# Kernel tuning notes

Measured on AMD Instinct MI355X. Metric: run time of the kernel, lower is better.

The kernel has to match this reference:

```python
import jax, jax.numpy as jnp
import numpy as np

EPS = 1e-6
NUM_HEADS = 16


def _layernorm(x, g, b):
    m = jnp.mean(x, axis=-1, keepdims=True)
    v = jnp.mean(jnp.square(x - m), axis=-1, keepdims=True)
    return (x - m) / jnp.sqrt(v + EPS) * g + b


def _rotate_half(x):
    x1, x2 = jnp.split(x, 2, axis=-1)
    return jnp.concatenate([-x2, x1], axis=-1)


def setup_inputs() -> dict:
    key = jax.random.key(0)
    B, N, C = 2, 2048, 1024
    H = NUM_HEADS
    D = C // H
    F = int(C * 4.0)
    ks = jax.random.split(key, 12)
    s = 0.02
    pos = jnp.arange(N)[:, None].astype(jnp.float32)
    inv_freq = 1.0 / (10000.0 ** (jnp.arange(0, D, 2, dtype=jnp.float32) / D))
    freqs = pos * inv_freq[None, :]          # [N, D/2]
    emb = jnp.concatenate([freqs, freqs], axis=-1)  # [N, D]
    return {
        "x": jax.random.normal(ks[0], (B, N, C), jnp.float32),
        "rotary_cos": jnp.cos(emb),
        "rotary_sin": jnp.sin(emb),
        "ln1_g": jnp.ones((C,), jnp.float32),
        "ln1_b": jnp.zeros((C,), jnp.float32),
        "Wq": jax.random.normal(ks[1], (C, C), jnp.float32) * s,
        "bq": jnp.zeros((C,), jnp.float32),
        "Wk": jax.random.normal(ks[2], (C, C), jnp.float32) * s,
        "bk": jnp.zeros((C,), jnp.float32),
        "Wv": jax.random.normal(ks[3], (C, C), jnp.float32) * s,
        "bv": jnp.zeros((C,), jnp.float32),
        "Wo": jax.random.normal(ks[4], (C, C), jnp.float32) * s,
        "bo": jnp.zeros((C,), jnp.float32),
        "ln2_g": jnp.ones((C,), jnp.float32),
        "ln2_b": jnp.zeros((C,), jnp.float32),
        "W1": jax.random.normal(ks[5], (F, C), jnp.float32) * s,
        "b1": jnp.zeros((F,), jnp.float32),
        "W2": jax.random.normal(ks[6], (C, F), jnp.float32) * s,
        "b2": jnp.zeros((C,), jnp.float32),
    }


def reference(x, rotary_cos, rotary_sin, ln1_g, ln1_b, Wq, bq, Wk, bk, Wv, bv,
              Wo, bo, ln2_g, ln2_b, W1, b1, W2, b2):
    B, N, C = x.shape
    H = NUM_HEADS
    D = C // H

    # --- attention branch ---
    h = _layernorm(x, ln1_g, ln1_b)
    q = (h @ Wq.T + bq).reshape(B, N, H, D).transpose(0, 2, 1, 3)  # [B,H,N,D]
    k = (h @ Wk.T + bk).reshape(B, N, H, D).transpose(0, 2, 1, 3)
    v = (h @ Wv.T + bv).reshape(B, N, H, D).transpose(0, 2, 1, 3)

    cos = rotary_cos[None, None, :, :]  # [1,1,N,D]
    sin = rotary_sin[None, None, :, :]
    q = q * cos + _rotate_half(q) * sin
    k = k * cos + _rotate_half(k) * sin

    scale = D ** -0.5
    attn = jnp.einsum('bhnd,bhmd->bhnm', q, k) * scale
    attn = jax.nn.softmax(attn, axis=-1)
    out = jnp.einsum('bhnm,bhmd->bhnd', attn, v)
    out = out.transpose(0, 2, 1, 3).reshape(B, N, C)
    out = out @ Wo.T + bo
    x = x + out

    # --- MLP branch ---
    h = _layernorm(x, ln2_g, ln2_b)
    h = jax.nn.gelu(h @ W1.T + b1, approximate=False)  # torch nn.GELU exact
    h = h @ W2.T + b2
    return x + h
```

## Files before the change

kernel.cpp:

```cpp
#include <hip/hip_runtime.h>
#include <hip/hip_bf16.h>

#define B_ 2
#define N_ 2048
#define C_ 1024
#define H_ 16
#define D_ 64
#define F_ 4096
#define M_ 4096

typedef __attribute__((ext_vector_type(8))) short bf16x8;
typedef __attribute__((ext_vector_type(4))) float f32x4;

__device__ inline unsigned short f2bf(float f) {
  unsigned int u = __float_as_uint(f);
  u = (u + 0x7FFFu + ((u >> 16) & 1u)) >> 16;
  return (unsigned short)u;
}
__device__ inline float bf2f(unsigned short u) {
  unsigned int x = ((unsigned int)u) << 16;
  return __uint_as_float(x);
}

__global__ __launch_bounds__(256)
void cvt_all(const float4* __restrict__ s0, const float4* __restrict__ s1,
             const float4* __restrict__ s2, const float4* __restrict__ s3,
             const float4* __restrict__ s4, const float4* __restrict__ s5,
             ushort4* __restrict__ d0, ushort4* __restrict__ d1,
             ushort4* __restrict__ d2, ushort4* __restrict__ d3,
             ushort4* __restrict__ d4, ushort4* __restrict__ d5) {
  int b = blockIdx.x;
  const float4* s; ushort4* d; int i;
  if      (b < 1024) { s = s0; d = d0; i = b * 256 + threadIdx.x; }
  else if (b < 2048) { s = s1; d = d1; i = (b - 1024) * 256 + threadIdx.x; }
  else if (b < 3072) { s = s2; d = d2; i = (b - 2048) * 256 + threadIdx.x; }
  else if (b < 4096) { s = s3; d = d3; i = (b - 3072) * 256 + threadIdx.x; }
  else if (b < 8192) { s = s4; d = d4; i = (b - 4096) * 256 + threadIdx.x; }
  else               { s = s5; d = d5; i = (b - 8192) * 256 + threadIdx.x; }
  float4 f = s[i];
  ushort4 o;
  o.x = f2bf(f.x); o.y = f2bf(f.y); o.z = f2bf(f.z); o.w = f2bf(f.w);
  d[i] = o;
}

__global__ __launch_bounds__(256)
void ln_kernel(const float* __restrict__ x, const float* __restrict__ g,
               const float* __restrict__ b, unsigned short* __restrict__ out) {
  __shared__ float red[8];
  const int row = blockIdx.x;
  const int t = threadIdx.x;
  const float4 xv = *(const float4*)(x + row * 1024 + t * 4);
  float s  = xv.x + xv.y + xv.z + xv.w;
  float sq = xv.x * xv.x + xv.y * xv.y + xv.z * xv.z + xv.w * xv.w;
  #pragma unroll
  for (int off = 32; off >= 1; off >>= 1) {
    s  += __shfl_down(s, off);
    sq += __shfl_down(sq, off);
  }
  const int lane = t & 63, wave = t >> 6;
  if (lane == 0) { red[wave * 2] = s; red[wave * 2 + 1] = sq; }
  __syncthreads();
  float ts = red[0] + red[2] + red[4] + red[6];
  float tq = red[1] + red[3] + red[5] + red[7];
  float mean = ts * (1.0f / 1024.0f);
  float var  = tq * (1.0f / 1024.0f) - mean * mean;
  float rstd = rsqrtf(var + 1e-6f);
  float xs[4] = {xv.x, xv.y, xv.z, xv.w};
  #pragma unroll
  for (int i = 0; i < 4; i++) {
    int c = t * 4 + i;
    float y = (xs[i] - mean) * rstd * g[c] + b[c];
    out[row * 1024 + c] = f2bf(y);
  }
}

__global__ __launch_bounds__(256)
void add_bias(const float* __restrict__ resid, const float* __restrict__ bias,
              float* __restrict__ out) {
  const int i = (blockIdx.x * 256 + threadIdx.x) * 4;
  const int col = i & 1023;
  float4 r = *(const float4*)(resid + i);
  float4 b = *(const float4*)(bias + col);
  float4 o;
  o.x = r.x + b.x; o.y = r.y + b.y; o.z = r.z + b.z; o.w = r.w + b.w;
  *(float4*)(out + i) = o;
}

__global__ __launch_bounds__(512, 1)
void gemm_splitk(const unsigned short* __restrict__ A,
                 const unsigned short* __restrict__ Bw,
                 int Kfull, int ksplit,
                 float* __restrict__ out) {
  __shared__ unsigned short sA[2][256 * 64];
  __shared__ unsigned short sB[2][128 * 64];
  const int t = threadIdx.x;
  const int wave = t >> 6, lane = t & 63;
  const int quad = lane >> 4, l16 = lane & 15;
  const int wm = (wave >> 1) * 64, wn = (wave & 1) * 64;
  const int id = blockIdx.x;
  const int xcd = id & 7, r_ = id >> 3;
  const int m_blk = xcd * 2 + (r_ & 1);
  const int cu = r_ >> 1;
  const int n_blk = cu & 7;
  const int split = cu >> 3;
  const int m0 = m_blk * 256, n0 = n_blk * 128;
  const int k0base = split * ksplit;

  f32x4 acc[4][4];
  #pragma unroll
  for (int i = 0; i < 4; i++)
    #pragma unroll
    for (int j = 0; j < 4; j++) acc[i][j] = (f32x4){0.f, 0.f, 0.f, 0.f};

  const int sc = (((t & 7) ^ ((t >> 3) & 7)) * 8);
  const unsigned short* gA = A  + (long)(m0 + (t >> 3)) * Kfull + k0base + sc;
  const unsigned short* gB = Bw + (long)(n0 + (t >> 3)) * Kfull + k0base + sc;

  auto stage_pair = [&](int k0, int buf, int pr) {
    if (pr < 2) {
      #pragma unroll
      for (int i = pr * 2; i < pr * 2 + 2; i++)
        __builtin_amdgcn_global_load_lds((const unsigned int*)(gA + (long)(64 * i) * Kfull + k0),
                                         (unsigned int*)(&sA[buf][i * 4096 + wave * 8 * 64]), 16, 0, 0);
    } else {
      #pragma unroll
      for (int i = 0; i < 2; i++)
        __builtin_amdgcn_global_load_lds((const unsigned int*)(gB + (long)(64 * i) * Kfull + k0),
                                         (unsigned int*)(&sB[buf][i * 4096 + wave * 8 * 64]), 16, 0, 0);
    }
  };

  stage_pair(0, 0, 0); stage_pair(0, 0, 1); stage_pair(0, 0, 2);
  stage_pair(64, 1, 0);
  asm volatile("s_waitcnt vmcnt(2)" ::: "memory");
  __builtin_amdgcn_s_barrier();

  const int so0 = ((quad ^ (l16 & 7)) * 8);
  const int so1 = (((4 + quad) ^ (l16 & 7)) * 8);

  const int nk = ksplit >> 6;
  for (int t_ = 0; t_ < nk; t_++) {
    const int R = t_ & 1;
    const unsigned short* rA = sA[R];
    const unsigned short* rB = sB[R];
    {
      bf16x8 af[4], bfr[4];
      #pragma unroll
      for (int ii = 0; ii < 4; ii++)
        af[ii] = *(const bf16x8*)(&rA[(wm + ii * 16 + l16) * 64 + so0]);
      #pragma unroll
      for (int j = 0; j < 4; j++)
        bfr[j] = *(const bf16x8*)(&rB[(wn + j * 16 + l16) * 64 + so0]);
      if (t_ + 1 < nk) stage_pair((t_ + 1) * 64, R ^ 1, 1);
      __builtin_amdgcn_s_barrier();
      asm volatile("s_waitcnt lgkmcnt(0)" ::: "memory");
      __builtin_amdgcn_sched_barrier(0);
      __builtin_amdgcn_s_setprio(1);
      #pragma unroll
      for (int ii = 0; ii < 4; ii++)
        #pragma unroll
        for (int j = 0; j < 4; j++)
          acc[ii][j] = __builtin_amdgcn_mfma_f32_16x16x32_bf16(af[ii], bfr[j], acc[ii][j], 0, 0, 0);
      __builtin_amdgcn_s_setprio(0);
      __builtin_amdgcn_s_barrier();
    }
    {
      bf16x8 af[4], bfr[4];
      #pragma unroll
      for (int ii = 0; ii < 4; ii++)
        af[ii] = *(const bf16x8*)(&rA[(wm + ii * 16 + l16) * 64 + so1]);
      #pragma unroll
      for (int j = 0; j < 4; j++)
        bfr[j] = *(const bf16x8*)(&rB[(wn + j * 16 + l16) * 64 + so1]);
      if (t_ + 1 < nk) stage_pair((t_ + 1) * 64, R ^ 1, 2);
      __builtin_amdgcn_s_barrier();
      asm volatile("s_waitcnt lgkmcnt(0)" ::: "memory");
      __builtin_amdgcn_sched_barrier(0);
      __builtin_amdgcn_s_setprio(1);
      #pragma unroll
      for (int ii = 0; ii < 4; ii++)
        #pragma unroll
        for (int j = 0; j < 4; j++)
          acc[ii][j] = __builtin_amdgcn_mfma_f32_16x16x32_bf16(af[ii], bfr[j], acc[ii][j], 0, 0, 0);
      __builtin_amdgcn_s_setprio(0);
    }
    __builtin_amdgcn_s_barrier();
    if (t_ + 2 < nk) {
      stage_pair((t_ + 2) * 64, R, 0);
      asm volatile("s_waitcnt vmcnt(2)" ::: "memory");
      __builtin_amdgcn_s_barrier();
    } else if (t_ + 1 < nk) {
      asm volatile("s_waitcnt vmcnt(0)" ::: "memory");
      __builtin_amdgcn_s_barrier();
    }
  }

  #pragma unroll
  for (int ii = 0; ii < 4; ii++) {
    #pragma unroll
    for (int j = 0; j < 4; j++) {
      int col = n0 + wn + j * 16 + l16;
      #pragma unroll
      for (int r = 0; r < 4; r++) {
        int row = m0 + wm + ii * 16 + quad * 4 + r;
        unsafeAtomicAdd(&out[row * 1024 + col], acc[ii][j][r]);
      }
    }
  }
}

template<int EPI>
__global__ __launch_bounds__(512, 1)
void gemm256(const unsigned short* __restrict__ A,
             const unsigned short* __restrict__ Bw,
             const float* __restrict__ bias,
             const float* __restrict__ bq, const float* __restrict__ bk,
             const float* __restrict__ bv,
             const float* __restrict__ rc, const float* __restrict__ rs,
             unsigned short* __restrict__ o0,
             unsigned short* __restrict__ ko, unsigned short* __restrict__ vt) {
  const int K = 1024;
  __shared__ unsigned short sA[2][256 * 64];
  __shared__ unsigned short sB[2][256 * 64];
  const int t = threadIdx.x;
  const int wave = t >> 6, lane = t & 63;
  const int quad = lane >> 4, l16 = lane & 15;
  const int wm = (wave & 1) * 128, wn = (wave >> 1) * 64;
  const int id = blockIdx.x;
  const int xcd = id & 7, r_ = id >> 3;
  int m_blk, n_blk;
  if (EPI == 0) { n_blk = xcd * 2 + (r_ >> 4); m_blk = r_ & 15; }
  else          { m_blk = xcd * 2 + r_ / 12;   n_blk = r_ % 12; }
  const int m0 = m_blk * 256, n0 = n_blk * 256;

  f32x4 acc[8][4];
  #pragma unroll
  for (int i = 0; i < 8; i++)
    #pragma unroll
    for (int j = 0; j < 4; j++) acc[i][j] = (f32x4){0.f, 0.f, 0.f, 0.f};

  const int sc = (((t & 7) ^ ((t >> 3) & 7)) * 8);
  const unsigned short* gA = A  + (m0 + (t >> 3)) * K + sc;
  const unsigned short* gB = Bw + (n0 + (t >> 3)) * K + sc;

  auto stage_pair = [&](int k0, int buf, int pr) {
    if (pr < 2) {
      unsigned short* lA = &sA[buf][(wave * 8) * 64];
      #pragma unroll
      for (int r = pr * 2; r < pr * 2 + 2; r++)
        __builtin_amdgcn_global_load_lds((const unsigned int*)(gA + (64 * r) * K + k0),
                                         (unsigned int*)(lA + 64 * r * 64), 16, 0, 0);
    } else {
      unsigned short* lB = &sB[buf][(wave * 8) * 64];
      #pragma unroll
      for (int r = (pr - 2) * 2; r < (pr - 2) * 2 + 2; r++)
        __builtin_amdgcn_global_load_lds((const unsigned int*)(gB + (64 * r) * K + k0),
                                         (unsigned int*)(lB + 64 * r * 64), 16, 0, 0);
    }
  };

  stage_pair(0, 0, 0); stage_pair(0, 0, 1); stage_pair(0, 0, 2); stage_pair(0, 0, 3);
  stage_pair(64, 1, 0);
  asm volatile("s_waitcnt vmcnt(2)" ::: "memory");
  __builtin_amdgcn_s_barrier();

  const int so0 = ((quad ^ (l16 & 7)) * 8);
  const int so1 = (((4 + quad) ^ (l16 & 7)) * 8);

  const int nk = K >> 6;
  for (int t_ = 0; t_ < nk; t_++) {
    const int R = t_ & 1;
    const unsigned short* rA = sA[R];
    const unsigned short* rB = sB[R];
    #pragma unroll
    for (int p = 0; p < 4; p++) {
      const int kk = p >> 1, ih = p & 1;
      const int so = kk ? so1 : so0;
      bf16x8 af[4], bfr[4];
      #pragma unroll
      for (int ii = 0; ii < 4; ii++)
        af[ii] = *(const bf16x8*)(&rA[(wm + (ih * 4 + ii) * 16 + l16) * 64 + so]);
      #pragma unroll
      for (int j = 0; j < 4; j++)
        bfr[j] = *(const bf16x8*)(&rB[(wn + j * 16 + l16) * 64 + so]);
      if (p < 3 && t_ + 1 < nk) stage_pair((t_ + 1) * 64, R ^ 1, p + 1);
      __builtin_amdgcn_s_barrier();
      asm volatile("s_waitcnt lgkmcnt(0)" ::: "memory");
      __builtin_amdgcn_sched_barrier(0);
      __builtin_amdgcn_s_setprio(1);
      #pragma unroll
      for (int ii = 0; ii < 4; ii++)
        #pragma unroll
        for (int j = 0; j < 4; j++)
          acc[ih * 4 + ii][j] =
              __builtin_amdgcn_mfma_f32_16x16x32_bf16(af[ii], bfr[j], acc[ih * 4 + ii][j], 0, 0, 0);
      __builtin_amdgcn_s_setprio(0);
      if (p < 3) __builtin_amdgcn_s_barrier();
    }
    __builtin_amdgcn_s_barrier();
    if (t_ + 2 < nk) {
      stage_pair((t_ + 2) * 64, R, 0);
      asm volatile("s_waitcnt vmcnt(2)" ::: "memory");
      __builtin_amdgcn_s_barrier();
    } else if (t_ + 1 < nk) {
      asm volatile("s_waitcnt vmcnt(0)" ::: "memory");
      __builtin_amdgcn_s_barrier();
    }
  }

  if (EPI == 0) {
    #pragma unroll
    for (int i = 0; i < 8; i++) {
      #pragma unroll
      for (int j = 0; j < 4; j++) {
        int col = n0 + wn + j * 16 + l16;
        float bb = bias[col];
        #pragma unroll
        for (int r = 0; r < 4; r++) {
          int row = m0 + wm + i * 16 + quad * 4 + r;
          float v = acc[i][j][r] + bb;
          float w = v * (1.0f + 0.044715f * v * v);
          float gl = v / (1.0f + __expf(-1.5957691216f * w));
          o0[row * 4096 + col] = f2bf(gl);
        }
      }
    }
  } else {
    const int rgn = n_blk >> 2;
    const int c0 = (n_blk & 3) * 256;
    if (rgn == 2) {
      #pragma unroll
      for (int i = 0; i < 8; i++) {
        int row0 = m0 + wm + i * 16 + quad * 4;
        int bidx = row0 >> 11, n0r = row0 & 2047;
        #pragma unroll
        for (int j = 0; j < 4; j++) {
          int d = j * 16 + l16;
          int c = c0 + wn + d;
          int h = c >> 6;
          float bb = bv[c];
          __hip_bfloat162 p01 = __float22bfloat162_rn(float2{acc[i][j][0] + bb, acc[i][j][1] + bb});
          __hip_bfloat162 p23 = __float22bfloat162_rn(float2{acc[i][j][2] + bb, acc[i][j][3] + bb});
          unsigned int u01, u23;
          __builtin_memcpy(&u01, &p01, 4);
          __builtin_memcpy(&u23, &p23, 4);
          *(uint2*)(vt + (((bidx * 16 + h) * 64) + d) * 2048 + n0r) = make_uint2(u01, u23);
        }
      }
    } else {
      const float* bia = (rgn == 0) ? bq : bk;
      unsigned short* outp = (rgn == 0) ? o0 : ko;
      #pragma unroll
      for (int i = 0; i < 8; i++) {
        #pragma unroll
        for (int r = 0; r < 4; r++) {
          int row = m0 + wm + i * 16 + quad * 4 + r;
          int bidx = row >> 11, n = row & 2047;
          #pragma unroll
          for (int j = 0; j < 4; j++) {
            int d = j * 16 + l16;
            int c = c0 + wn + d;
            int h = c >> 6;
            int oi = ((bidx * 16 + h) * 2048 + n) * 64 + d;
            float val = acc[i][j][r] + bia[c];
            float pv  = acc[i][j ^ 2][r] + bia[c ^ 32];
            float rot = (j < 2) ? -pv : pv;
            float y = val * rc[n * 64 + d] + rot * rs[n * 64 + d];
            if (rgn == 0) y *= 0.125f;
            outp[oi] = f2bf(y);
          }
        }
      }
    }
  }
}

__global__ __launch_bounds__(512)
void flash_attn(const unsigned short* __restrict__ q,
                const unsigned short* __restrict__ k,
                const unsigned short* __restrict__ vt,
                unsigned short* __restrict__ o0h,
                unsigned short* __restrict__ o1h,
                float* __restrict__ l0g, float* __restrict__ l1g) {
  __shared__ unsigned short sK[2][64 * 64];
  __shared__ unsigned short sVt[2][64 * 64];
  __shared__ unsigned short sPt[2][8][16 * 72];
  const int t = threadIdx.x;
  const int wave = t >> 6, lane = t & 63;
  const int quad = lane >> 4, l16 = lane & 15;
  const int id = blockIdx.x;
  const int bh = (id & 7) * 4 + ((id >> 3) & 3);
  const int qb = (id >> 5) & 7;
  const int kvh = id >> 8;
  const int base = bh * (N_ * D_);

  bf16x8 qa[2][2];
  #pragma unroll
  for (int qt = 0; qt < 2; qt++) {
    int qrow = qb * 256 + wave * 32 + qt * 16 + l16;
    #pragma unroll
    for (int kk = 0; kk < 2; kk++)
      qa[qt][kk] = *(const bf16x8*)(q + base + qrow * D_ + kk * 32 + quad * 8);
  }
  float l_i[2] = {0.f, 0.f};
  f32x4 o_acc[2][4];
  #pragma unroll
  for (int qt = 0; qt < 2; qt++)
    #pragma unroll
    for (int dt = 0; dt < 4; dt++) o_acc[qt][dt] = (f32x4){0.f, 0.f, 0.f, 0.f};

  const int sc = (((t & 7) ^ ((t >> 3) & 7)) * 8);
  const unsigned short* gK  = k  + base + (t >> 3) * 64 + sc;
  const unsigned short* gVt = vt + bh * (64 * 2048) + (t >> 3) * 2048 + sc;

  auto stage = [&](int kt, int buf) {
    __builtin_amdgcn_global_load_lds((const unsigned int*)(gK + kt * 64 * 64),
                                     (unsigned int*)(&sK[buf][(wave * 8) * 64]), 16, 0, 0);
    __builtin_amdgcn_global_load_lds((const unsigned int*)(gVt + kt * 64),
                                     (unsigned int*)(&sVt[buf][(wave * 8) * 64]), 16, 0, 0);
  };
  const int kt0 = kvh * 16, kt1 = kt0 + 16;
  stage(kt0, 0);
  __syncthreads();

  const int so0 = ((quad ^ (l16 & 7)) * 8);
  const int so1 = (((4 + quad) ^ (l16 & 7)) * 8);

  for (int kt = kt0; kt < kt1; kt++) {
    const int cur = kt & 1;
    if (kt + 1 < kt1) stage(kt + 1, cur ^ 1);

    f32x4 s_acc[2][4];
    #pragma unroll
    for (int nt = 0; nt < 4; nt++) {
      bf16x8 kb0 = *(const bf16x8*)(&sK[cur][(nt * 16 + l16) * 64 + so0]);
      bf16x8 kb1 = *(const bf16x8*)(&sK[cur][(nt * 16 + l16) * 64 + so1]);
      #pragma unroll
      for (int qt = 0; qt < 2; qt++) {
        f32x4 a = (f32x4){0.f, 0.f, 0.f, 0.f};
        a = __builtin_amdgcn_mfma_f32_16x16x32_bf16(kb0, qa[qt][0], a, 0, 0, 0);
        a = __builtin_amdgcn_mfma_f32_16x16x32_bf16(kb1, qa[qt][1], a, 0, 0, 0);
        s_acc[qt][nt] = a;
      }
    }
    #pragma unroll
    for (int qt = 0; qt < 2; qt++) {
      float rsum = 0.f;
      #pragma unroll
      for (int nt = 0; nt < 4; nt++)
        #pragma unroll
        for (int r = 0; r < 4; r++) {
          float p = __expf(s_acc[qt][nt][r]);
          s_acc[qt][nt][r] = p;
          rsum += p;
        }
      rsum += __shfl_xor(rsum, 16);
      rsum += __shfl_xor(rsum, 32);
      l_i[qt] += rsum;
      #pragma unroll
      for (int nt = 0; nt < 4; nt++) {
        __hip_bfloat162 p01 = __float22bfloat162_rn(float2{s_acc[qt][nt][0], s_acc[qt][nt][1]});
        __hip_bfloat162 p23 = __float22bfloat162_rn(float2{s_acc[qt][nt][2], s_acc[qt][nt][3]});
        unsigned int u01, u23;
        __builtin_memcpy(&u01, &p01, 4);
        __builtin_memcpy(&u23, &p23, 4);
        *(uint2*)(&sPt[qt][wave][l16 * 72 + nt * 16 + quad * 4]) = make_uint2(u01, u23);
      }
    }
    __asm__ volatile("s_waitcnt lgkmcnt(0)" ::: "memory");
    bf16x8 pt[2][2];
    #pragma unroll
    for (int qt = 0; qt < 2; qt++) {
      pt[qt][0] = *(const bf16x8*)(&sPt[qt][wave][l16 * 72 + quad * 8]);
      pt[qt][1] = *(const bf16x8*)(&sPt[qt][wave][l16 * 72 + 32 + quad * 8]);
    }
    #pragma unroll
    for (int dt = 0; dt < 4; dt++) {
      int d0 = dt * 16 + l16;
      bf16x8 va0 = *(const bf16x8*)(&sVt[cur][d0 * 64 + so0]);
      bf16x8 va1 = *(const bf16x8*)(&sVt[cur][d0 * 64 + so1]);
      #pragma unroll
      for (int qt = 0; qt < 2; qt++) {
        o_acc[qt][dt] = __builtin_amdgcn_mfma_f32_16x16x32_bf16(va0, pt[qt][0], o_acc[qt][dt], 0, 0, 0);
        o_acc[qt][dt] = __builtin_amdgcn_mfma_f32_16x16x32_bf16(va1, pt[qt][1], o_acc[qt][dt], 0, 0, 0);
      }
    }
    __syncthreads();
  }

  unsigned short* op = kvh ? o1h : o0h;
  float* lp = kvh ? l1g : l0g;
  const int b = bh >> 4, h = bh & 15;
  #pragma unroll
  for (int qt = 0; qt < 2; qt++) {
    const int qrow = qb * 256 + wave * 32 + qt * 16 + l16;
    if (quad == 0) lp[bh * 2048 + qrow] = l_i[qt];
    const int tok = b * N_ + qrow;
    #pragma unroll
    for (int dt = 0; dt < 4; dt++) {
      __hip_bfloat162 p01 = __float22bfloat162_rn(float2{o_acc[qt][dt][0], o_acc[qt][dt][1]});
      __hip_bfloat162 p23 = __float22bfloat162_rn(float2{o_acc[qt][dt][2], o_acc[qt][dt][3]});
      unsigned int u01, u23;
      __builtin_memcpy(&u01, &p01, 4);
      __builtin_memcpy(&u23, &p23, 4);
      int col = h * 64 + dt * 16 + quad * 4;
      *(uint2*)(op + tok * C_ + col) = make_uint2(u01, u23);
    }
  }
}

__global__ __launch_bounds__(256)
void attn_norm(const unsigned short* __restrict__ o0h,
               const unsigned short* __restrict__ o1h,
               const float* __restrict__ l0g, const float* __restrict__ l1g,
               unsigned short* __restrict__ o) {
  const int i = (blockIdx.x * 256 + threadIdx.x) * 8;
  const int row = i >> 10, c = i & 1023;
  const int h = c >> 6;
  const int b = row >> 11, n = row & 2047;
  const int li = (b * 16 + h) * 2048 + n;
  const float inv = 1.0f / (l0g[li] + l1g[li]);
  ushort4 a0 = *(const ushort4*)(o0h + i);
  ushort4 a1 = *(const ushort4*)(o0h + i + 4);
  ushort4 b0 = *(const ushort4*)(o1h + i);
  ushort4 b1 = *(const ushort4*)(o1h + i + 4);
  ushort4 r0, r1;
  r0.x = f2bf((bf2f(a0.x) + bf2f(b0.x)) * inv);
  r0.y = f2bf((bf2f(a0.y) + bf2f(b0.y)) * inv);
  r0.z = f2bf((bf2f(a0.z) + bf2f(b0.z)) * inv);
  r0.w = f2bf((bf2f(a0.w) + bf2f(b0.w)) * inv);
  r1.x = f2bf((bf2f(a1.x) + bf2f(b1.x)) * inv);
  r1.y = f2bf((bf2f(a1.y) + bf2f(b1.y)) * inv);
  r1.z = f2bf((bf2f(a1.z) + bf2f(b1.z)) * inv);
  r1.w = f2bf((bf2f(a1.w) + bf2f(b1.w)) * inv);
  *(ushort4*)(o + i) = r0;
  *(ushort4*)(o + i + 4) = r1;
}

extern "C" void kernel_launch(void* const* d_in, const int* in_sizes, int n_in,
                              void* d_out, int out_size, void* d_ws, size_t ws_size,
                              hipStream_t stream) {
  const float* x   = (const float*)d_in[0];
  const float* rc  = (const float*)d_in[1];
  const float* rs  = (const float*)d_in[2];
  const float* g1  = (const float*)d_in[3];
  const float* be1 = (const float*)d_in[4];
  const float* Wq  = (const float*)d_in[5];
  const float* bq  = (const float*)d_in[6];
  const float* Wk  = (const float*)d_in[7];
  const float* bk  = (const float*)d_in[8];
  const float* Wv  = (const float*)d_in[9];
  const float* bv  = (const float*)d_in[10];
  const float* Wo  = (const float*)d_in[11];
  const float* bo  = (const float*)d_in[12];
  const float* g2  = (const float*)d_in[13];
  const float* be2 = (const float*)d_in[14];
  const float* W1  = (const float*)d_in[15];
  const float* b1m = (const float*)d_in[16];
  const float* W2  = (const float*)d_in[17];
  const float* b2m = (const float*)d_in[18];
  float* out = (float*)d_out;

  char* ws = (char*)d_ws;
  unsigned short* wqkv = (unsigned short*)(ws + 0);
  unsigned short* wo   = (unsigned short*)(ws + 6291456);
  unsigned short* w1   = (unsigned short*)(ws + 8388608);
  unsigned short* w2   = (unsigned short*)(ws + 16777216);
  unsigned short* h1   = (unsigned short*)(ws + 25165824);
  unsigned short* qa   = (unsigned short*)(ws + 33554432);
  unsigned short* ka   = (unsigned short*)(ws + 41943040);
  unsigned short* va   = (unsigned short*)(ws + 50331648);
  unsigned short* ao   = (unsigned short*)(ws + 58720256);
  float*          x1   = (float*)(ws + 67108864);
  float*          l0   = (float*)(ws + 67108864);
  float*          l1   = l0 + 65536;
  unsigned short* u    = (unsigned short*)(ws + 33554432);

  cvt_all<<<12288, 256, 0, stream>>>(
      (const float4*)Wq, (const float4*)Wk, (const float4*)Wv, (const float4*)Wo,
      (const float4*)W1, (const float4*)W2,
      (ushort4*)wqkv, (ushort4*)(wqkv + 1048576), (ushort4*)(wqkv + 2097152),
      (ushort4*)wo, (ushort4*)w1, (ushort4*)w2);

  ln_kernel<<<4096, 256, 0, stream>>>(x, g1, be1, h1);
  gemm256<1><<<192, 512, 0, stream>>>(h1, wqkv, nullptr, bq, bk, bv, rc, rs, qa, ka, va);
  flash_attn<<<512, 512, 0, stream>>>(qa, ka, va, ao, h1, l0, l1);
  attn_norm<<<2048, 256, 0, stream>>>(ao, h1, l0, l1, ao);
  add_bias<<<4096, 256, 0, stream>>>(x, bo, x1);
  gemm_splitk<<<256, 512, 0, stream>>>(ao, wo, 1024, 512, x1);
  ln_kernel<<<4096, 256, 0, stream>>>(x1, g2, be2, h1);
  gemm256<0><<<256, 512, 0, stream>>>(h1, w1, b1m, nullptr, nullptr, nullptr, nullptr, nullptr,
                                      u, nullptr, nullptr);
  add_bias<<<4096, 256, 0, stream>>>(x1, b2m, out);
  gemm_splitk<<<256, 512, 0, stream>>>(u, w2, 4096, 2048, out);
}
```

Measured before the change: 412.4 us.

## Enlarge split-K GEMM tile to 256x256 with more K splits

The split-K GEMM used for the Wo and W2 projections now uses a 256x256 output tile instead of 256x128, with each wave computing 128x64. The K dimension is split four ways instead of two, so the grid stays at 256 blocks. The larger tile gives more MFMA work per shared-memory load and better operand reuse. In exchange it doubles the number of fp32 atomic adds into the output, increases accumulator register pressure (32 f32x4 accumulators per thread), and doubles shared memory for B.

```diff
diff --git a/kernel.cpp b/kernel.cpp
--- a/kernel.cpp
+++ b/kernel.cpp
@@ -87,50 +87,52 @@
 }
 
 __global__ __launch_bounds__(512, 1)
-void gemm_splitk(const unsigned short* __restrict__ A,
-                 const unsigned short* __restrict__ Bw,
-                 int Kfull, int ksplit,
-                 float* __restrict__ out) {
+void gemm256_sk(const unsigned short* __restrict__ A,
+                const unsigned short* __restrict__ Bw,
+                int Kfull, int ksplit,
+                float* __restrict__ out) {
   __shared__ unsigned short sA[2][256 * 64];
-  __shared__ unsigned short sB[2][128 * 64];
+  __shared__ unsigned short sB[2][256 * 64];
   const int t = threadIdx.x;
   const int wave = t >> 6, lane = t & 63;
   const int quad = lane >> 4, l16 = lane & 15;
-  const int wm = (wave >> 1) * 64, wn = (wave & 1) * 64;
+  const int wm = (wave & 1) * 128, wn = (wave >> 1) * 64;
   const int id = blockIdx.x;
   const int xcd = id & 7, r_ = id >> 3;
   const int m_blk = xcd * 2 + (r_ & 1);
-  const int cu = r_ >> 1;
-  const int n_blk = cu & 7;
-  const int split = cu >> 3;
-  const int m0 = m_blk * 256, n0 = n_blk * 128;
+  const int rest = r_ >> 1;
+  const int n_blk = rest & 3;
+  const int split = rest >> 2;
+  const int m0 = m_blk * 256, n0 = n_blk * 256;
   const int k0base = split * ksplit;
 
-  f32x4 acc[4][4];
-  #pragma unroll
-  for (int i = 0; i < 4; i++)
+  f32x4 acc[8][4];
+  #pragma unroll
+  for (int i = 0; i < 8; i++)
     #pragma unroll
     for (int j = 0; j < 4; j++) acc[i][j] = (f32x4){0.f, 0.f, 0.f, 0.f};
 
   const int sc = (((t & 7) ^ ((t >> 3) & 7)) * 8);
-  const unsigned short* gA = A  + (long)(m0 + (t >> 3)) * Kfull + k0base + sc;
-  const unsigned short* gB = Bw + (long)(n0 + (t >> 3)) * Kfull + k0base + sc;
+  const unsigned short* gA = A  + (m0 + (t >> 3)) * Kfull + k0base + sc;
+  const unsigned short* gB = Bw + (n0 + (t >> 3)) * Kfull + k0base + sc;
 
   auto stage_pair = [&](int k0, int buf, int pr) {
     if (pr < 2) {
-      #pragma unroll
-      for (int i = pr * 2; i < pr * 2 + 2; i++)
-        __builtin_amdgcn_global_load_lds((const unsigned int*)(gA + (long)(64 * i) * Kfull + k0),
-                                         (unsigned int*)(&sA[buf][i * 4096 + wave * 8 * 64]), 16, 0, 0);
+      unsigned short* lA = &sA[buf][(wave * 8) * 64];
+      #pragma unroll
+      for (int r = pr * 2; r < pr * 2 + 2; r++)
+        __builtin_amdgcn_global_load_lds((const unsigned int*)(gA + (64 * r) * Kfull + k0),
+                                         (unsigned int*)(lA + 64 * r * 64), 16, 0, 0);
     } else {
-      #pragma unroll
-      for (int i = 0; i < 2; i++)
-        __builtin_amdgcn_global_load_lds((const unsigned int*)(gB + (long)(64 * i) * Kfull + k0),
-                                         (unsigned int*)(&sB[buf][i * 4096 + wave * 8 * 64]), 16, 0, 0);
+      unsigned short* lB = &sB[buf][(wave * 8) * 64];
+      #pragma unroll
+      for (int r = (pr - 2) * 2; r < (pr - 2) * 2 + 2; r++)
+        __builtin_amdgcn_global_load_lds((const unsigned int*)(gB + (64 * r) * Kfull + k0),
+                                         (unsigned int*)(lB + 64 * r * 64), 16, 0, 0);
     }
   };
 
-  stage_pair(0, 0, 0); stage_pair(0, 0, 1); stage_pair(0, 0, 2);
+  stage_pair(0, 0, 0); stage_pair(0, 0, 1); stage_pair(0, 0, 2); stage_pair(0, 0, 3);
   stage_pair(64, 1, 0);
   asm volatile("s_waitcnt vmcnt(2)" ::: "memory");
   __builtin_amdgcn_s_barrier();
@@ -143,15 +145,18 @@
     const int R = t_ & 1;
     const unsigned short* rA = sA[R];
     const unsigned short* rB = sB[R];
-    {
+    #pragma unroll
+    for (int p = 0; p < 4; p++) {
+      const int kk = p >> 1, ih = p & 1;
+      const int so = kk ? so1 : so0;
       bf16x8 af[4], bfr[4];
       #pragma unroll
       for (int ii = 0; ii < 4; ii++)
-        af[ii] = *(const bf16x8*)(&rA[(wm + ii * 16 + l16) * 64 + so0]);
+        af[ii] = *(const bf16x8*)(&rA[(wm + (ih * 4 + ii) * 16 + l16) * 64 + so]);
       #pragma unroll
       for (int j = 0; j < 4; j++)
-        bfr[j] = *(const bf16x8*)(&rB[(wn + j * 16 + l16) * 64 + so0]);
-      if (t_ + 1 < nk) stage_pair((t_ + 1) * 64, R ^ 1, 1);
+        bfr[j] = *(const bf16x8*)(&rB[(wn + j * 16 + l16) * 64 + so]);
+      if (p < 3 && t_ + 1 < nk) stage_pair((t_ + 1) * 64, R ^ 1, p + 1);
       __builtin_amdgcn_s_barrier();
       asm volatile("s_waitcnt lgkmcnt(0)" ::: "memory");
       __builtin_amdgcn_sched_barrier(0);
@@ -160,29 +165,10 @@
       for (int ii = 0; ii < 4; ii++)
         #pragma unroll
         for (int j = 0; j < 4; j++)
-          acc[ii][j] = __builtin_amdgcn_mfma_f32_16x16x32_bf16(af[ii], bfr[j], acc[ii][j], 0, 0, 0);
+          acc[ih * 4 + ii][j] =
+              __builtin_amdgcn_mfma_f32_16x16x32_bf16(af[ii], bfr[j], acc[ih * 4 + ii][j], 0, 0, 0);
       __builtin_amdgcn_s_setprio(0);
-      __builtin_amdgcn_s_barrier();
-    }
-    {
-      bf16x8 af[4], bfr[4];
-      #pragma unroll
-      for (int ii = 0; ii < 4; ii++)
-        af[ii] = *(const bf16x8*)(&rA[(wm + ii * 16 + l16) * 64 + so1]);
-      #pragma unroll
-      for (int j = 0; j < 4; j++)
-        bfr[j] = *(const bf16x8*)(&rB[(wn + j * 16 + l16) * 64 + so1]);
-      if (t_ + 1 < nk) stage_pair((t_ + 1) * 64, R ^ 1, 2);
-      __builtin_amdgcn_s_barrier();
-      asm volatile("s_waitcnt lgkmcnt(0)" ::: "memory");
-      __builtin_amdgcn_sched_barrier(0);
-      __builtin_amdgcn_s_setprio(1);
-      #pragma unroll
-      for (int ii = 0; ii < 4; ii++)
-        #pragma unroll
-        for (int j = 0; j < 4; j++)
-          acc[ii][j] = __builtin_amdgcn_mfma_f32_16x16x32_bf16(af[ii], bfr[j], acc[ii][j], 0, 0, 0);
-      __builtin_amdgcn_s_setprio(0);
+      if (p < 3) __builtin_amdgcn_s_barrier();
     }
     __builtin_amdgcn_s_barrier();
     if (t_ + 2 < nk) {
@@ -196,7 +182,7 @@
   }
 
   #pragma unroll
-  for (int ii = 0; ii < 4; ii++) {
+  for (int ii = 0; ii < 8; ii++) {
     #pragma unroll
     for (int j = 0; j < 4; j++) {
       int col = n0 + wn + j * 16 + l16;
@@ -587,10 +573,10 @@
   flash_attn<<<512, 512, 0, stream>>>(qa, ka, va, ao, h1, l0, l1);
   attn_norm<<<2048, 256, 0, stream>>>(ao, h1, l0, l1, ao);
   add_bias<<<4096, 256, 0, stream>>>(x, bo, x1);
-  gemm_splitk<<<256, 512, 0, stream>>>(ao, wo, 1024, 512, x1);
+  gemm256_sk<<<256, 512, 0, stream>>>(ao, wo, 1024, 256, x1);
   ln_kernel<<<4096, 256, 0, stream>>>(x1, g2, be2, h1);
   gemm256<0><<<256, 512, 0, stream>>>(h1, w1, b1m, nullptr, nullptr, nullptr, nullptr, nullptr,
                                       u, nullptr, nullptr);
   add_bias<<<4096, 256, 0, stream>>>(x1, b2m, out);
-  gemm_splitk<<<256, 512, 0, stream>>>(u, w2, 4096, 2048, out);
-}
+  gemm256_sk<<<256, 512, 0, stream>>>(u, w2, 4096, 1024, out);
+}
```

Measured after the change: 453.1 us. 9.9% more time.
